# Kernel tuning notes

Hardware: AMD Instinct MI355X
Metric: run time of the kernel (lower is better)

## Reference

```python
import jax, jax.numpy as jnp
import numpy as np

N_NODES = 10000
N_EDGES = 160000
N_REL = 4
N_GRAPHS = 256
IN_DIM = 64


def rgcn_layer(x, W, root, bias, src, dst, etype, num_nodes, num_rel):
    # PyG RGCNConv with default aggr='mean': per-relation mean aggregation,
    # plus root transform and bias.
    h = jnp.einsum('nd,rdf->rnf', x, W)            # [R, N, F] grouped GEMM
    msg = h[etype, src]                             # [E, F] gather per edge
    comb = dst * num_rel + etype                    # (dst, relation) bucket
    cnt = jax.ops.segment_sum(jnp.ones(etype.shape, x.dtype), comb,
                              num_segments=num_nodes * num_rel)
    inv = 1.0 / jnp.maximum(cnt, 1.0)
    msg = msg * inv[comb][:, None]                  # per-relation mean norm
    agg = jax.ops.segment_sum(msg, dst, num_segments=num_nodes)  # scatter-add
    return agg + x @ root + bias


def global_mean_pool(x, batch, num_graphs):
    s = jax.ops.segment_sum(x, batch, num_segments=num_graphs)
    c = jax.ops.segment_sum(jnp.ones(batch.shape, x.dtype), batch,
                            num_segments=num_graphs)
    return s / jnp.maximum(c, 1.0)[:, None]


def setup_inputs() -> dict:
    key = jax.random.key(0)
    ks = jax.random.split(key, 20)
    s = 0.02
    inp = {
        'x': jax.random.normal(ks[0], (N_NODES, IN_DIM), jnp.float32),
        'edge_index': jax.random.randint(ks[1], (2, N_EDGES), 0, N_NODES),
        'edge_type': jax.random.randint(ks[2], (N_EDGES,), 0, N_REL),
        'batch': jnp.sort(jax.random.randint(ks[3], (N_NODES,), 0, N_GRAPHS)),
        'W1': jax.random.normal(ks[4], (N_REL, IN_DIM, 1024), jnp.float32) * s,
        'root1': jax.random.normal(ks[5], (IN_DIM, 1024), jnp.float32) * s,
        'b1': jnp.zeros((1024,), jnp.float32),
        'W2': jax.random.normal(ks[6], (N_REL, 1024, 1024), jnp.float32) * s,
        'root2': jax.random.normal(ks[7], (1024, 1024), jnp.float32) * s,
        'b2': jnp.zeros((1024,), jnp.float32),
        'W3': jax.random.normal(ks[8], (N_REL, 1024, 712), jnp.float32) * s,
        'root3': jax.random.normal(ks[9], (1024, 712), jnp.float32) * s,
        'b3': jnp.zeros((712,), jnp.float32),
        'fw1': jax.random.normal(ks[10], (712, 64), jnp.float32) * s,
        'fb1': jnp.zeros((64,), jnp.float32),
        'fw2': jax.random.normal(ks[11], (64, 1), jnp.float32) * s,
        'fb2': jnp.zeros((1,), jnp.float32),
    }
    return inp


def reference(x, edge_index, edge_type, batch, W1, root1, b1, W2, root2, b2,
              W3, root3, b3, fw1, fb1, fw2, fb2):
    src, dst = edge_index[0], edge_index[1]
    # dropout is a no-op in eval mode (training=False)
    h = jax.nn.relu(rgcn_layer(x, W1, root1, b1, src, dst, edge_type, N_NODES, N_REL))
    h = jax.nn.relu(rgcn_layer(h, W2, root2, b2, src, dst, edge_type, N_NODES, N_REL))
    h = jax.nn.relu(rgcn_layer(h, W3, root3, b3, src, dst, edge_type, N_NODES, N_REL))
    g = global_mean_pool(h, batch, N_GRAPHS)        # [G, 712]
    g = jax.nn.relu(g @ fw1 + fb1)
    out = g @ fw2 + fb2                             # [G, 1]
    return out
```

## Files before the change

### kernel.cpp

```cpp
#include <hip/hip_runtime.h>
#include <stdint.h>

#define N_NODES 10000
#define N_EDGES 160000
#define N_REL   4
#define N_GRAPHS 256
#define NBUCKET (N_NODES * N_REL)

typedef __attribute__((ext_vector_type(8))) short short8;
typedef __attribute__((ext_vector_type(4))) float float4v;

__device__ __forceinline__ unsigned short f2bf(float f) {
  unsigned int u = __float_as_uint(f);
  u = u + 0x7FFFu + ((u >> 16) & 1u);
  return (unsigned short)(u >> 16);
}
__device__ __forceinline__ float bf2f(unsigned short b) {
  return __uint_as_float(((unsigned int)b) << 16);
}

__device__ __forceinline__ void g2lds16(const void* g, void* l) {
  __builtin_amdgcn_global_load_lds(
      (const __attribute__((address_space(1))) void*)g,
      (__attribute__((address_space(3))) void*)l, 16, 0, 0);
}

__device__ __forceinline__ int lower_bound_i(const int* a, int n, int key) {
  int lo = 0, hi = n;
  while (lo < hi) { int mid = (lo + hi) >> 1; if (a[mid] < key) lo = mid + 1; else hi = mid; }
  return lo;
}

__global__ void count_edges_k(const int* __restrict__ ei, const int* __restrict__ et,
                              int* __restrict__ cnt, int E) {
  int e = blockIdx.x * 256 + threadIdx.x;
  if (e < E) atomicAdd(&cnt[ei[E + e] * N_REL + et[e]], 1);
}

__global__ void scan_block_k(const int* __restrict__ cnt, int* __restrict__ eexcl,
                             int* __restrict__ btot, int n) {
  int i = blockIdx.x * 256 + threadIdx.x;
  int v = (i < n) ? cnt[i] : 0;
  int lane = threadIdx.x & 63, wv = threadIdx.x >> 6;
  int s = v;
  #pragma unroll
  for (int off = 1; off < 64; off <<= 1) {
    int t = __shfl_up(s, off, 64);
    if (lane >= off) s += t;
  }
  __shared__ int wt[4];
  if (lane == 63) wt[wv] = s;
  __syncthreads();
  int wadd = 0;
  for (int w = 0; w < wv; ++w) wadd += wt[w];
  int incl = s + wadd;
  if (i < n) eexcl[i] = incl - v;
  if (threadIdx.x == 255) btot[blockIdx.x] = incl;
}

__global__ void scan_final_k(const int* __restrict__ cnt, const int* __restrict__ eexcl,
                             const int* __restrict__ btot, int* __restrict__ offs,
                             int* __restrict__ cursor, float* __restrict__ inv, int n) {
  __shared__ int wred[4];
  __shared__ int sboff;
  int t = threadIdx.x;
  int part = (t < (int)blockIdx.x) ? btot[t] : 0;
  #pragma unroll
  for (int off = 32; off > 0; off >>= 1) part += __shfl_down(part, off, 64);
  if ((t & 63) == 0) wred[t >> 6] = part;
  __syncthreads();
  if (t == 0) sboff = wred[0] + wred[1] + wred[2] + wred[3];
  __syncthreads();
  int i = blockIdx.x * 256 + t;
  if (i < n) {
    int o = sboff + eexcl[i];
    offs[i] = o;
    cursor[i] = o;
    int c = cnt[i];
    inv[i] = 1.0f / (float)(c > 1 ? c : 1);
  }
}

__global__ void fill_csr_k(const int* __restrict__ ei, const int* __restrict__ et,
                           int* __restrict__ cursor, int* __restrict__ elist, int E) {
  int e = blockIdx.x * 256 + threadIdx.x;
  if (e >= E) return;
  int dst = ei[E + e], src = ei[e], r = et[e];
  int pos = atomicAdd(&cursor[dst * N_REL + r], 1);
  elist[pos] = src;
}

__global__ void wcat_transpose_k(const float* __restrict__ W, const float* __restrict__ root,
                                 unsigned short* __restrict__ out, int Din4, int F, int K) {
  __shared__ float tile[32][33];
  int kb = blockIdx.x * 32, fb = blockIdx.y * 32;
  for (int i = threadIdx.y; i < 32; i += 8) {
    int k = kb + i, f = fb + threadIdx.x;
    float v = 0.0f;
    if (k < K && f < F) v = (k < Din4) ? W[(size_t)k * F + f] : root[(size_t)(k - Din4) * F + f];
    tile[i][threadIdx.x] = v;
  }
  __syncthreads();
  for (int i = threadIdx.y; i < 32; i += 8) {
    int f = fb + i, k = kb + threadIdx.x;
    if (f < F && k < K) out[(size_t)f * K + k] = f2bf(tile[threadIdx.x][i]);
  }
}

__global__ void aggregate64_k(const float* __restrict__ x, const int* __restrict__ offs,
                              const int* __restrict__ cnt, const float* __restrict__ inv,
                              const int* __restrict__ elist, unsigned short* __restrict__ Xcat) {
  const int n = blockIdx.x;
  const int wv = threadIdx.x >> 6;
  const int col = threadIdx.x & 63;
  const int b = n * N_REL + wv;
  const int start = offs[b], c = cnt[b];
  const float sc = inv[b];
  float acc = 0.0f;
  for (int j = 0; j < c; ++j) {
    int s = elist[start + j];
    acc += x[(size_t)s * 64 + col];
  }
  Xcat[(size_t)n * 320 + wv * 64 + col] = f2bf(acc * sc);
  if (wv == 0)
    Xcat[(size_t)n * 320 + 256 + col] = f2bf(x[(size_t)n * 64 + col]);
}

__global__ void aggregate_bf16_k(const unsigned short* __restrict__ h,
                                 const int* __restrict__ offs, const int* __restrict__ cnt,
                                 const float* __restrict__ inv, const int* __restrict__ elist,
                                 unsigned short* __restrict__ Xcat) {
  const int n = blockIdx.x;
  const int tid = threadIdx.x;
  const int K5 = 5120, Din = 1024;
  __shared__ int sid[256];
  for (int r = 0; r < N_REL; ++r) {
    int b = n * N_REL + r;
    int start = offs[b], c = cnt[b];
    float sc = inv[b];
    float a0 = 0.f, a1 = 0.f, a2 = 0.f, a3 = 0.f;
    for (int base = 0; base < c; base += 256) {
      int m = min(256, c - base);
      __syncthreads();
      if (tid < m) sid[tid] = elist[start + base + tid];
      __syncthreads();
      for (int j = 0; j < m; ++j) {
        ushort4 v = *(const ushort4*)(h + (size_t)sid[j] * Din + tid * 4);
        a0 += bf2f(v.x); a1 += bf2f(v.y); a2 += bf2f(v.z); a3 += bf2f(v.w);
      }
    }
    ushort4 o;
    o.x = f2bf(a0 * sc); o.y = f2bf(a1 * sc); o.z = f2bf(a2 * sc); o.w = f2bf(a3 * sc);
    *(ushort4*)&Xcat[(size_t)n * K5 + r * Din + tid * 4] = o;
  }
  *(ushort4*)&Xcat[(size_t)n * K5 + 4 * Din + tid * 4] =
      *(const ushort4*)(h + (size_t)n * Din + tid * 4);
}

__global__ __launch_bounds__(256) void gemm_bt_bias_relu_k(
    const short* __restrict__ A, const short* __restrict__ Bt,
    const float* __restrict__ bias, unsigned short* __restrict__ C,
    int M, int Ndim, int K) {
  __shared__ short As[128 * 64];
  __shared__ short Bs[128 * 64];

  const int tid = threadIdx.x;
  const int wave = tid >> 6;
  const int lane = tid & 63;
  const int mBase = blockIdx.y * 128;
  const int nBase = blockIdx.x * 128;
  const int half = lane >> 4;
  const int lrow = lane & 15;
  const int wm = (wave >> 1) * 64;
  const int wn = (wave & 1) * 64;
  const int srow = lane >> 3;
  const int schunk = (lane & 7) ^ srow;

  float4v acc[4][4] = {};

  for (int k0 = 0; k0 < K; k0 += 64) {
    #pragma unroll
    for (int p = 0; p < 4; ++p) {
      int rb = wave * 32 + p * 8;
      int r = rb + srow;
      int gr = mBase + r; if (gr > M - 1) gr = M - 1;
      g2lds16(A + (size_t)gr * K + k0 + schunk * 8, &As[rb * 64]);
      int gn = nBase + r; if (gn > Ndim - 1) gn = Ndim - 1;
      g2lds16(Bt + (size_t)gn * K + k0 + schunk * 8, &Bs[rb * 64]);
    }
    __syncthreads();

    #pragma unroll
    for (int kk = 0; kk < 2; ++kk) {
      short8 a[4], b[4];
      #pragma unroll
      for (int i = 0; i < 4; ++i) {
        int r = wm + i * 16 + lrow;
        int q = (kk * 4 + half) ^ (r & 7);
        a[i] = *(const short8*)&As[r * 64 + q * 8];
      }
      #pragma unroll
      for (int j = 0; j < 4; ++j) {
        int r = wn + j * 16 + lrow;
        int q = (kk * 4 + half) ^ (r & 7);
        b[j] = *(const short8*)&Bs[r * 64 + q * 8];
      }
      #pragma unroll
      for (int i = 0; i < 4; ++i)
        #pragma unroll
        for (int j = 0; j < 4; ++j)
          acc[i][j] = __builtin_amdgcn_mfma_f32_16x16x32_bf16(a[i], b[j], acc[i][j], 0, 0, 0);
    }
    __syncthreads();
  }

  #pragma unroll
  for (int i = 0; i < 4; ++i) {
    int row0 = mBase + wm + i * 16 + half * 4;
    #pragma unroll
    for (int j = 0; j < 4; ++j) {
      int col = nBase + wn + j * 16 + lrow;
      if (col < Ndim) {
        float bv = bias[col];
        #pragma unroll
        for (int r = 0; r < 4; ++r) {
          int rr = row0 + r;
          if (rr < M) C[(size_t)rr * Ndim + col] = f2bf(fmaxf(acc[i][j][r] + bv, 0.0f));
        }
      }
    }
  }
}

__global__ __launch_bounds__(256) void pool_mlp_k(
    const unsigned short* __restrict__ h, const int* __restrict__ batch,
    const float* __restrict__ fw1, const float* __restrict__ fb1,
    const float* __restrict__ fw2, const float* __restrict__ fb2,
    float* __restrict__ out, int N, int F) {
  __shared__ float gsh[712];
  __shared__ float part[4][64];

  const int gid = blockIdx.x;
  const int tid = threadIdx.x;
  const int lo = lower_bound_i(batch, N, gid);
  const int hi = lower_bound_i(batch, N, gid + 1);
  const float scale = (hi > lo) ? 1.0f / (float)(hi - lo) : 0.0f;
  const int C4 = F >> 2;

  if (tid < C4) {
    float a0 = 0.f, a1 = 0.f, a2 = 0.f, a3 = 0.f;
    for (int n = lo; n < hi; ++n) {
      ushort4 v = *(const ushort4*)(h + (size_t)n * F + tid * 4);
      a0 += bf2f(v.x); a1 += bf2f(v.y); a2 += bf2f(v.z); a3 += bf2f(v.w);
    }
    gsh[tid * 4 + 0] = a0 * scale;
    gsh[tid * 4 + 1] = a1 * scale;
    gsh[tid * 4 + 2] = a2 * scale;
    gsh[tid * 4 + 3] = a3 * scale;
  }
  __syncthreads();

  const int f = tid & 63;
  const int wv = tid >> 6;
  const int d0 = wv * 178;
  const int d1 = min(d0 + 178, F);
  float a = 0.0f;
  int d = d0;
  for (; d + 3 < d1; d += 4) {
    float g0 = gsh[d], g1 = gsh[d + 1], g2 = gsh[d + 2], g3 = gsh[d + 3];
    a += g0 * fw1[(size_t)d * 64 + f]
       + g1 * fw1[(size_t)(d + 1) * 64 + f]
       + g2 * fw1[(size_t)(d + 2) * 64 + f]
       + g3 * fw1[(size_t)(d + 3) * 64 + f];
  }
  for (; d < d1; ++d) a += gsh[d] * fw1[(size_t)d * 64 + f];
  part[wv][f] = a;
  __syncthreads();

  if (tid < 64) {
    float hsum = part[0][tid] + part[1][tid] + part[2][tid] + part[3][tid] + fb1[tid];
    hsum = fmaxf(hsum, 0.0f);
    float p = hsum * fw2[tid];
    #pragma unroll
    for (int off = 32; off > 0; off >>= 1) p += __shfl_down(p, off, 64);
    if (tid == 0) out[gid] = p + fb2[0];
  }
}

extern "C" void kernel_launch(void* const* d_in, const int* in_sizes, int n_in,
                              void* d_out, int out_size, void* d_ws, size_t ws_size,
                              hipStream_t stream) {
  (void)in_sizes; (void)n_in; (void)out_size;
  const float* x    = (const float*)d_in[0];
  const int*  ei    = (const int*)d_in[1];
  const int*  et    = (const int*)d_in[2];
  const int*  batch = (const int*)d_in[3];
  const float* W1 = (const float*)d_in[4],  *root1 = (const float*)d_in[5],  *b1 = (const float*)d_in[6];
  const float* W2 = (const float*)d_in[7],  *root2 = (const float*)d_in[8],  *b2 = (const float*)d_in[9];
  const float* W3 = (const float*)d_in[10], *root3 = (const float*)d_in[11], *b3 = (const float*)d_in[12];
  const float* fw1 = (const float*)d_in[13], *fb1 = (const float*)d_in[14];
  const float* fw2 = (const float*)d_in[15], *fb2 = (const float*)d_in[16];
  float* out = (float*)d_out;

  char* ws = (char*)d_ws;
  size_t off = 0;
  auto alloc = [&](size_t bytes) -> void* {
    void* p = ws + off; off += (bytes + 255) & ~(size_t)255; return p;
  };
  int*   cnt    = (int*)alloc(NBUCKET * 4);
  int*   offs   = (int*)alloc(NBUCKET * 4);
  int*   cursor = (int*)alloc(NBUCKET * 4);
  int*   eexcl  = (int*)alloc(NBUCKET * 4);
  int*   btot   = (int*)alloc(256 * 4);
  int*   elist  = (int*)alloc(N_EDGES * 4);
  float* inv    = (float*)alloc(NBUCKET * 4);
  unsigned short* Xcat  = (unsigned short*)alloc((size_t)N_NODES * 5120 * 2);
  unsigned short* WcatT = (unsigned short*)alloc((size_t)1024 * 5120 * 2);
  unsigned short* hA = (unsigned short*)alloc((size_t)N_NODES * 1024 * 2);
  unsigned short* hB = (unsigned short*)alloc((size_t)N_NODES * 1024 * 2);
  (void)ws_size;

  hipMemsetAsync(cnt, 0, NBUCKET * 4, stream);
  count_edges_k<<<(N_EDGES + 255) / 256, 256, 0, stream>>>(ei, et, cnt, N_EDGES);
  int nsb = (NBUCKET + 255) / 256;
  scan_block_k<<<nsb, 256, 0, stream>>>(cnt, eexcl, btot, NBUCKET);
  scan_final_k<<<nsb, 256, 0, stream>>>(cnt, eexcl, btot, offs, cursor, inv, NBUCKET);
  fill_csr_k<<<(N_EDGES + 255) / 256, 256, 0, stream>>>(ei, et, cursor, elist, N_EDGES);

  wcat_transpose_k<<<dim3(10, 32), dim3(32, 8), 0, stream>>>(W1, root1, WcatT, 256, 1024, 320);
  aggregate64_k<<<N_NODES, 256, 0, stream>>>(x, offs, cnt, inv, elist, Xcat);
  gemm_bt_bias_relu_k<<<dim3(8, 79), 256, 0, stream>>>(
      (const short*)Xcat, (const short*)WcatT, b1, hA, N_NODES, 1024, 320);

  wcat_transpose_k<<<dim3(160, 32), dim3(32, 8), 0, stream>>>(W2, root2, WcatT, 4096, 1024, 5120);
  aggregate_bf16_k<<<N_NODES, 256, 0, stream>>>(hA, offs, cnt, inv, elist, Xcat);
  gemm_bt_bias_relu_k<<<dim3(8, 79), 256, 0, stream>>>(
      (const short*)Xcat, (const short*)WcatT, b2, hB, N_NODES, 1024, 5120);

  wcat_transpose_k<<<dim3(160, 23), dim3(32, 8), 0, stream>>>(W3, root3, WcatT, 4096, 712, 5120);
  aggregate_bf16_k<<<N_NODES, 256, 0, stream>>>(hB, offs, cnt, inv, elist, Xcat);
  gemm_bt_bias_relu_k<<<dim3(6, 79), 256, 0, stream>>>(
      (const short*)Xcat, (const short*)WcatT, b3, hA, N_NODES, 712, 5120);

  pool_mlp_k<<<N_GRAPHS, 256, 0, stream>>>(hA, batch, fw1, fb1, fw2, fb2, out,
                                           N_NODES, 712);
}
```

Baseline: 602.6 us.

## Split aggregation into per-chunk wavefronts and remap GEMM tiles per XCD

The bf16 aggregation kernel now runs one 64-thread wavefront per (node, 256-column chunk) and processes all four relation buckets in one pass over the contiguous edge list. Fewer syncs and more independent blocks should help latency hiding. The GEMM switches to a 1D grid whose block index is remapped so that consecutive tiles in M land on the same XCD, to improve L2 reuse of A/B tiles across the eight chiplets. The grid is padded to 80 row tiles, so extra blocks with out-of-range M rely on the existing row clamping and store guards.

```diff
diff --git a/kernel.cpp b/kernel.cpp
--- a/kernel.cpp
+++ b/kernel.cpp
@@ -126,49 +126,78 @@
     Xcat[(size_t)n * 320 + 256 + col] = f2bf(x[(size_t)n * 64 + col]);
 }
 
-__global__ void aggregate_bf16_k(const unsigned short* __restrict__ h,
-                                 const int* __restrict__ offs, const int* __restrict__ cnt,
-                                 const float* __restrict__ inv, const int* __restrict__ elist,
-                                 unsigned short* __restrict__ Xcat) {
-  const int n = blockIdx.x;
-  const int tid = threadIdx.x;
-  const int K5 = 5120, Din = 1024;
-  __shared__ int sid[256];
+__global__ __launch_bounds__(64) void aggregate_bf16_k(
+    const unsigned short* __restrict__ h,
+    const int* __restrict__ offs, const int* __restrict__ cnt,
+    const float* __restrict__ inv, const int* __restrict__ elist,
+    unsigned short* __restrict__ Xcat) {
+  const int bid = blockIdx.x;
+  const int chunk = (bid & 7) >> 1;
+  const int n = ((bid >> 3) << 1) | (bid & 1);
+  const int lane = threadIdx.x;
+  const int col = chunk * 256 + lane * 4;
+  const int Din = 1024, K5 = 5120;
+  const int b0 = n * N_REL;
+  const int start = offs[b0];
+  const int c0 = cnt[b0], c1 = cnt[b0 + 1], c2 = cnt[b0 + 2], c3 = cnt[b0 + 3];
+  int pr[5];
+  pr[0] = 0; pr[1] = c0; pr[2] = pr[1] + c1; pr[3] = pr[2] + c2; pr[4] = pr[3] + c3;
+  const int cTot = pr[4];
+
+  float ax[4] = {0.f, 0.f, 0.f, 0.f};
+  float ay[4] = {0.f, 0.f, 0.f, 0.f};
+  float az[4] = {0.f, 0.f, 0.f, 0.f};
+  float aw[4] = {0.f, 0.f, 0.f, 0.f};
+
+  __shared__ int sid[64];
+  for (int base = 0; base < cTot; base += 64) {
+    int m = min(64, cTot - base);
+    __syncthreads();
+    if (lane < m) sid[lane] = elist[start + base + lane];
+    __syncthreads();
+    #pragma unroll
+    for (int r = 0; r < N_REL; ++r) {
+      int lo = max(pr[r] - base, 0);
+      int hi = min(pr[r + 1] - base, m);
+      for (int j = lo; j < hi; ++j) {
+        ushort4 v = *(const ushort4*)(h + (size_t)sid[j] * Din + col);
+        ax[r] += bf2f(v.x); ay[r] += bf2f(v.y);
+        az[r] += bf2f(v.z); aw[r] += bf2f(v.w);
+      }
+    }
+  }
+
+  #pragma unroll
   for (int r = 0; r < N_REL; ++r) {
-    int b = n * N_REL + r;
-    int start = offs[b], c = cnt[b];
-    float sc = inv[b];
-    float a0 = 0.f, a1 = 0.f, a2 = 0.f, a3 = 0.f;
-    for (int base = 0; base < c; base += 256) {
-      int m = min(256, c - base);
-      __syncthreads();
-      if (tid < m) sid[tid] = elist[start + base + tid];
-      __syncthreads();
-      for (int j = 0; j < m; ++j) {
-        ushort4 v = *(const ushort4*)(h + (size_t)sid[j] * Din + tid * 4);
-        a0 += bf2f(v.x); a1 += bf2f(v.y); a2 += bf2f(v.z); a3 += bf2f(v.w);
-      }
-    }
+    float sc = inv[b0 + r];
     ushort4 o;
-    o.x = f2bf(a0 * sc); o.y = f2bf(a1 * sc); o.z = f2bf(a2 * sc); o.w = f2bf(a3 * sc);
-    *(ushort4*)&Xcat[(size_t)n * K5 + r * Din + tid * 4] = o;
-  }
-  *(ushort4*)&Xcat[(size_t)n * K5 + 4 * Din + tid * 4] =
-      *(const ushort4*)(h + (size_t)n * Din + tid * 4);
+    o.x = f2bf(ax[r] * sc); o.y = f2bf(ay[r] * sc);
+    o.z = f2bf(az[r] * sc); o.w = f2bf(aw[r] * sc);
+    *(ushort4*)&Xcat[(size_t)n * K5 + r * Din + col] = o;
+  }
+  *(ushort4*)&Xcat[(size_t)n * K5 + 4 * Din + col] =
+      *(const ushort4*)(h + (size_t)n * Din + col);
 }
 
 __global__ __launch_bounds__(256) void gemm_bt_bias_relu_k(
     const short* __restrict__ A, const short* __restrict__ Bt,
     const float* __restrict__ bias, unsigned short* __restrict__ C,
-    int M, int Ndim, int K) {
+    int M, int Ndim, int K, int NX) {
   __shared__ short As[128 * 64];
   __shared__ short Bs[128 * 64];
+
+  const int bid = blockIdx.x;
+  const int xcd = bid & 7;
+  const int local = bid >> 3;
+  const int t = xcd * (NX * 10) + local;
+  const int tileM = t / NX;
+  const int tileN = t - tileM * NX;
+  const int mBase = tileM * 128;
+  const int nBase = tileN * 128;
 
   const int tid = threadIdx.x;
   const int wave = tid >> 6;
   const int lane = tid & 63;
-  const int mBase = blockIdx.y * 128;
-  const int nBase = blockIdx.x * 128;
   const int half = lane >> 4;
   const int lrow = lane & 15;
   const int wm = (wave >> 1) * 64;
@@ -329,18 +358,18 @@
 
   wcat_transpose_k<<<dim3(10, 32), dim3(32, 8), 0, stream>>>(W1, root1, WcatT, 256, 1024, 320);
   aggregate64_k<<<N_NODES, 256, 0, stream>>>(x, offs, cnt, inv, elist, Xcat);
-  gemm_bt_bias_relu_k<<<dim3(8, 79), 256, 0, stream>>>(
-      (const short*)Xcat, (const short*)WcatT, b1, hA, N_NODES, 1024, 320);
+  gemm_bt_bias_relu_k<<<8 * 80, 256, 0, stream>>>(
+      (const short*)Xcat, (const short*)WcatT, b1, hA, N_NODES, 1024, 320, 8);
 
   wcat_transpose_k<<<dim3(160, 32), dim3(32, 8), 0, stream>>>(W2, root2, WcatT, 4096, 1024, 5120);
-  aggregate_bf16_k<<<N_NODES, 256, 0, stream>>>(hA, offs, cnt, inv, elist, Xcat);
-  gemm_bt_bias_relu_k<<<dim3(8, 79), 256, 0, stream>>>(
-      (const short*)Xcat, (const short*)WcatT, b2, hB, N_NODES, 1024, 5120);
+  aggregate_bf16_k<<<N_NODES * 4, 64, 0, stream>>>(hA, offs, cnt, inv, elist, Xcat);
+  gemm_bt_bias_relu_k<<<8 * 80, 256, 0, stream>>>(
+      (const short*)Xcat, (const short*)WcatT, b2, hB, N_NODES, 1024, 5120, 8);
 
   wcat_transpose_k<<<dim3(160, 23), dim3(32, 8), 0, stream>>>(W3, root3, WcatT, 4096, 712, 5120);
-  aggregate_bf16_k<<<N_NODES, 256, 0, stream>>>(hB, offs, cnt, inv, elist, Xcat);
-  gemm_bt_bias_relu_k<<<dim3(6, 79), 256, 0, stream>>>(
-      (const short*)Xcat, (const short*)WcatT, b3, hA, N_NODES, 712, 5120);
+  aggregate_bf16_k<<<N_NODES * 4, 64, 0, stream>>>(hB, offs, cnt, inv, elist, Xcat);
+  gemm_bt_bias_relu_k<<<6 * 80, 256, 0, stream>>>(
+      (const short*)Xcat, (const short*)WcatT, b3, hA, N_NODES, 712, 5120, 6);
 
   pool_mlp_k<<<N_GRAPHS, 256, 0, stream>>>(hA, batch, fw1, fb1, fw2, fb2, out,
                                            N_NODES, 712);
```

New measurement: 551.5 us. -8.5%, faster.
